# Kernel tuning notes

Measured on AMD Instinct MI355X. Metric: run time of the kernel, lower is better.

Reference implementation:

```python
import jax, jax.numpy as jnp
import numpy as np

B, N, C = 64, 256, 1024
H = 16
D = C // H            # head_dim = 64
HALF = D // 2         # rope dim per axis = 32
PT = 16               # hw_seq_len
THETA = 10000.0


def build_rope_tables():
    # VisionRotaryEmbeddingFast: per-axis freqs, repeated r=2, 2D broadcat
    freqs = 1.0 / (THETA ** (np.arange(0, HALF, 2, dtype=np.float32) / HALF))  # [HALF/2]=16
    t = np.arange(PT, dtype=np.float32)                                        # ft==pt -> t=arange
    f = t[:, None] * freqs[None, :]                                            # [16,16]
    f = np.repeat(f, 2, axis=-1)                                               # [16,32]
    f2d = np.concatenate(
        [np.broadcast_to(f[:, None, :], (PT, PT, HALF)),
         np.broadcast_to(f[None, :, :], (PT, PT, HALF))], axis=-1)             # [16,16,64]
    f2d = f2d.reshape(PT * PT, D)                                              # [256,64]
    return jnp.asarray(np.cos(f2d)), jnp.asarray(np.sin(f2d))


def rotate_half(t):
    # (..., d) -> pairwise (x0,x1) -> (-x1, x0)
    t2 = t.reshape(*t.shape[:-1], -1, 2)
    return jnp.stack([-t2[..., 1], t2[..., 0]], axis=-1).reshape(t.shape)


def apply_rope(t, cos, sin):
    # t: [B,H,N,D]; cos/sin: [N,D]
    return t * cos + rotate_half(t) * sin


def setup_inputs() -> dict:
    key = jax.random.key(0)
    k1, k2, k3 = jax.random.split(key, 3)
    x = jax.random.normal(k1, (B, N, C), dtype=jnp.float32)
    mask = jnp.ones((1, 1, N, N), dtype=bool)  # True = attend (SDPA bool mask)
    qkv_w = jax.random.normal(k2, (3 * C, C), dtype=jnp.float32) * 0.02
    qkv_b = jnp.zeros((3 * C,), dtype=jnp.float32)
    proj_w = jax.random.normal(k3, (C, C), dtype=jnp.float32) * 0.02
    proj_b = jnp.zeros((C,), dtype=jnp.float32)
    rope_cos, rope_sin = build_rope_tables()
    return {"x": x, "mask": mask, "qkv_w": qkv_w, "qkv_b": qkv_b,
            "proj_w": proj_w, "proj_b": proj_b,
            "rope_cos": rope_cos, "rope_sin": rope_sin}


def reference(x, mask, qkv_w, qkv_b, proj_w, proj_b, rope_cos, rope_sin):
    b, n, c = x.shape
    scale = 1.0 / jnp.sqrt(jnp.asarray(D, x.dtype))
    qkv = x @ qkv_w.T + qkv_b                              # [B,N,3C]
    qkv = qkv.reshape(b, n, 3, H, D).transpose(2, 0, 3, 1, 4)  # [3,B,H,N,D]
    q, k, v = qkv[0], qkv[1], qkv[2]
    q = apply_rope(q, rope_cos, rope_sin)
    k = apply_rope(k, rope_cos, rope_sin)
    scores = jnp.einsum('bhnd,bhmd->bhnm', q, k) * scale   # [B,H,N,N]
    neg = jnp.asarray(jnp.finfo(scores.dtype).min, scores.dtype)
    scores = jnp.where(mask, scores, neg)
    attn = jax.nn.softmax(scores, axis=-1)
    out = jnp.einsum('bhnm,bhmd->bhnd', attn, v)           # [B,H,N,D]
    out = out.transpose(0, 2, 1, 3).reshape(b, n, c)       # [B,N,C]
    return out @ proj_w.T + proj_b
```

## Files before the change

### kernel.cpp

```cpp
#include <hip/hip_runtime.h>
#include <math.h>

typedef short s16x8 __attribute__((ext_vector_type(8)));
typedef float f32x4 __attribute__((ext_vector_type(4)));

#define DEV static __device__ __forceinline__

DEV unsigned short f2bf(float f){
  unsigned int u = __builtin_bit_cast(unsigned int, f);
  u += 0x7fffu + ((u >> 16) & 1u);
  return (unsigned short)(u >> 16);
}

DEV void gload_lds16(const void* g, void* l){
  __builtin_amdgcn_global_load_lds(
      (const __attribute__((address_space(1))) unsigned int*)g,
      (__attribute__((address_space(3))) unsigned int*)l,
      16, 0, 0);
}

DEV void stage_tile(const short* __restrict__ g, short* lds, int ld, int row0, int k0, int tid){
#pragma unroll
  for (int issue = 0; issue < 2; ++issue){
    int fi  = issue*256 + tid;
    int row = fi >> 2;
    int c8  = (fi & 3) * 8;
    const short* ga = g + (size_t)(row0 + row)*ld + k0 + c8;
    short* lb = lds + (size_t)(issue*256 + (tid & ~63))*8;
    gload_lds16(ga, lb);
  }
}

__global__ void cvt_bf16(const float* __restrict__ in, short* __restrict__ out, int n8){
  int i = blockIdx.x*blockDim.x + threadIdx.x;
  if (i >= n8) return;
  const float* p = in + (size_t)i*8;
  f32x4 a = *(const f32x4*)(p);
  f32x4 b = *(const f32x4*)(p+4);
  s16x8 o;
#pragma unroll
  for (int j=0;j<4;++j){ o[j] = (short)f2bf(a[j]); o[4+j] = (short)f2bf(b[j]); }
  *(s16x8*)(out + (size_t)i*8) = o;
}

template<int EPI>
__global__ __launch_bounds__(256)
void gemm_bt(const short* __restrict__ A, const short* __restrict__ Bw,
             const float* __restrict__ bias,
             const float* __restrict__ cosT, const float* __restrict__ sinT,
             short* __restrict__ q_out, short* __restrict__ k_out, short* __restrict__ v_out,
             float* __restrict__ f_out)
{
  constexpr int K = 1024;
  constexpr int NT = K/32;
  __shared__ short As[2][128*32];
  __shared__ short Bs[2][128*32];
  const int tid  = threadIdx.x;
  const int lane = tid & 63;
  const int wid  = tid >> 6;
  const int n0 = blockIdx.x * 128;
  const int m0 = blockIdx.y * 128;
  const int wr = (wid >> 1) * 64;
  const int wc = (wid & 1) * 64;
  const int lr = lane & 15;
  const int lk = lane >> 4;

  stage_tile(A,  As[0], K, m0, 0, tid);
  stage_tile(Bw, Bs[0], K, n0, 0, tid);
  asm volatile("s_waitcnt vmcnt(0)" ::: "memory");
  __syncthreads();

  f32x4 acc[4][4] = {};
  int cur = 0;
  for (int kt = 0; kt < NT; ++kt){
    if (kt + 1 < NT){
      stage_tile(A,  As[cur^1], K, m0, (kt+1)*32, tid);
      stage_tile(Bw, Bs[cur^1], K, n0, (kt+1)*32, tid);
    }
    s16x8 af[4], bf[4];
#pragma unroll
    for (int mi=0; mi<4; ++mi)
      af[mi] = *(const s16x8*)&As[cur][(wr + mi*16 + lr)*32 + lk*8];
#pragma unroll
    for (int ni=0; ni<4; ++ni)
      bf[ni] = *(const s16x8*)&Bs[cur][(wc + ni*16 + lr)*32 + lk*8];
#pragma unroll
    for (int mi=0; mi<4; ++mi)
#pragma unroll
      for (int ni=0; ni<4; ++ni)
        acc[mi][ni] = __builtin_amdgcn_mfma_f32_16x16x32_bf16(af[mi], bf[ni], acc[mi][ni], 0, 0, 0);
    asm volatile("s_waitcnt vmcnt(0)" ::: "memory");
    __syncthreads();
    cur ^= 1;
  }

  if constexpr (EPI == 0){
    const int sel = n0 >> 10;
#pragma unroll
    for (int mi=0; mi<4; ++mi){
#pragma unroll
      for (int ni=0; ni<4; ++ni){
        const int col  = n0 + wc + ni*16 + lr;
        const int rowb = m0 + wr + mi*16 + lk*4;
        const float bv = bias[col];
        const int rem = col & 1023;
        const int h = rem >> 6, d = rem & 63;
        if (sel < 2){
          short* dst = (sel == 0) ? q_out : k_out;
#pragma unroll
          for (int r=0; r<4; ++r){
            const int m = rowb + r;
            const int n = m & 255, b = m >> 8;
            float v = acc[mi][ni][r] + bv;
            float partner = __shfl_xor(v, 1, 64);
            float rot = (lane & 1) ? partner : -partner;
            float o = v * cosT[n*64 + d] + rot * sinT[n*64 + d];
            if (sel == 0) o *= 0.125f;
            dst[(((size_t)b*16 + h)*256 + n)*64 + d] = (short)f2bf(o);
          }
        } else {
          const int m = rowb;
          const int n = m & 255, b = m >> 8;
          unsigned long long pk = 0;
#pragma unroll
          for (int r=0; r<4; ++r)
            pk |= ((unsigned long long)f2bf(acc[mi][ni][r] + bv)) << (16*r);
          *(unsigned long long*)(v_out + (((size_t)b*16 + h)*64 + d)*256 + n) = pk;
        }
      }
    }
  } else {
#pragma unroll
    for (int mi=0; mi<4; ++mi){
#pragma unroll
      for (int ni=0; ni<4; ++ni){
        const int col  = n0 + wc + ni*16 + lr;
        const int rowb = m0 + wr + mi*16 + lk*4;
        const float bv = bias[col];
#pragma unroll
        for (int r=0; r<4; ++r)
          f_out[(size_t)(rowb + r)*1024 + col] = acc[mi][ni][r] + bv;
      }
    }
  }
}

__global__ __launch_bounds__(512)
void attn_kernel(const short* __restrict__ qh, const short* __restrict__ kh,
                 const short* __restrict__ vt, short* __restrict__ ao)
{
  __shared__ short Ks[256*64];
  __shared__ short Vs[64*256];
  __shared__ short Ps[8][32*64];
  const int tid  = threadIdx.x;
  const int lane = tid & 63;
  const int wid  = tid >> 6;
  const int lr   = lane & 15;
  const int lk   = lane >> 4;
  const int bh = blockIdx.x;
  const size_t base = (size_t)bh * 256 * 64;
  const short* Kg = kh + base;
  const short* Qg = qh + base;
  const short* Vg = vt + base;

#pragma unroll
  for (int p=0; p<4; ++p){
    int flat = (p*512 + tid)*8;
    uint4 kv = *(const uint4*)(Kg + flat);
    int krow = flat >> 6;  int kcb = (flat & 63)*2;
    *(uint4*)((char*)Ks + krow*128 + (kcb ^ ((krow&7)<<4))) = kv;
    uint4 vv = *(const uint4*)(Vg + flat);
    int vrow = flat >> 8;  int vcb = (flat & 255)*2;
    *(uint4*)((char*)Vs + vrow*512 + (vcb ^ ((vrow&7)<<4))) = vv;
  }

  const int qbase = wid*32;
  s16x8 qf[2][2];
#pragma unroll
  for (int qr=0; qr<2; ++qr)
#pragma unroll
    for (int ks=0; ks<2; ++ks)
      qf[qr][ks] = *(const s16x8*)(Qg + (size_t)(qbase + qr*16 + lr)*64 + ks*32 + lk*8);

  __syncthreads();

  float mrun[2][4], lrun[2][4];
  f32x4 o[2][4] = {};
#pragma unroll
  for (int qr=0; qr<2; ++qr)
#pragma unroll
    for (int r=0; r<4; ++r){ mrun[qr][r] = -INFINITY; lrun[qr][r] = 0.f; }

  for (int t=0; t<4; ++t){
    f32x4 s[2][4] = {};
#pragma unroll
    for (int kc=0; kc<4; ++kc){
      const int row = t*64 + kc*16 + lr;
#pragma unroll
      for (int ks=0; ks<2; ++ks){
        const int cb = ks*64 + lk*16;
        s16x8 kf = *(const s16x8*)((char*)Ks + row*128 + (cb ^ ((row&7)<<4)));
#pragma unroll
        for (int qr=0; qr<2; ++qr)
          s[qr][kc] = __builtin_amdgcn_mfma_f32_16x16x32_bf16(qf[qr][ks], kf, s[qr][kc], 0, 0, 0);
      }
    }
#pragma unroll
    for (int qr=0; qr<2; ++qr)
#pragma unroll
      for (int r=0; r<4; ++r){
        float mx = fmaxf(fmaxf(s[qr][0][r], s[qr][1][r]), fmaxf(s[qr][2][r], s[qr][3][r]));
        mx = fmaxf(mx, __shfl_xor(mx, 1, 64));
        mx = fmaxf(mx, __shfl_xor(mx, 2, 64));
        mx = fmaxf(mx, __shfl_xor(mx, 4, 64));
        mx = fmaxf(mx, __shfl_xor(mx, 8, 64));
        const float mnew  = fmaxf(mrun[qr][r], mx);
        const float alpha = __expf(mrun[qr][r] - mnew);
        float rsum = 0.f;
#pragma unroll
        for (int kc=0; kc<4; ++kc){
          float p = __expf(s[qr][kc][r] - mnew);
          s[qr][kc][r] = p;
          rsum += p;
        }
        rsum += __shfl_xor(rsum, 1, 64);
        rsum += __shfl_xor(rsum, 2, 64);
        rsum += __shfl_xor(rsum, 4, 64);
        rsum += __shfl_xor(rsum, 8, 64);
        lrun[qr][r] = lrun[qr][r]*alpha + rsum;
        mrun[qr][r] = mnew;
#pragma unroll
        for (int oc=0; oc<4; ++oc) o[qr][oc][r] *= alpha;
      }
#pragma unroll
    for (int qr=0; qr<2; ++qr)
#pragma unroll
      for (int kc=0; kc<4; ++kc)
#pragma unroll
        for (int r=0; r<4; ++r){
          const int row = qr*16 + lk*4 + r;
          const int cb  = (kc*16 + lr)*2;
          *(short*)((char*)&Ps[wid][0] + row*128 + (cb ^ ((row&7)<<4))) = (short)f2bf(s[qr][kc][r]);
        }
#pragma unroll
    for (int ks2=0; ks2<2; ++ks2){
      s16x8 pf[2];
#pragma unroll
      for (int qr=0; qr<2; ++qr){
        const int row = qr*16 + lr;
        const int cb  = ks2*64 + lk*16;
        pf[qr] = *(const s16x8*)((char*)&Ps[wid][0] + row*128 + (cb ^ ((row&7)<<4)));
      }
#pragma unroll
      for (int oc=0; oc<4; ++oc){
        const int vrow = oc*16 + lr;
        const int vcb  = t*128 + ks2*64 + lk*16;
        s16x8 vf = *(const s16x8*)((char*)Vs + vrow*512 + (vcb ^ ((vrow&7)<<4)));
#pragma unroll
        for (int qr=0; qr<2; ++qr)
          o[qr][oc] = __builtin_amdgcn_mfma_f32_16x16x32_bf16(pf[qr], vf, o[qr][oc], 0, 0, 0);
      }
    }
  }

  const int b = bh >> 4, h = bh & 15;
#pragma unroll
  for (int qr=0; qr<2; ++qr)
#pragma unroll
    for (int oc=0; oc<4; ++oc)
#pragma unroll
      for (int r=0; r<4; ++r){
        const int n = qbase + qr*16 + lk*4 + r;
        const int d = oc*16 + lr;
        float val = o[qr][oc][r] / lrun[qr][r];
        ao[(size_t)(b*256 + n)*1024 + h*64 + d] = (short)f2bf(val);
      }
}

extern "C" void kernel_launch(void* const* d_in, const int* in_sizes, int n_in,
                              void* d_out, int out_size, void* d_ws, size_t ws_size,
                              hipStream_t stream)
{
  const float* x      = (const float*)d_in[0];
  const float* qkv_w  = (const float*)d_in[2];
  const float* qkv_b  = (const float*)d_in[3];
  const float* proj_w = (const float*)d_in[4];
  const float* proj_b = (const float*)d_in[5];
  const float* rc     = (const float*)d_in[6];
  const float* rs     = (const float*)d_in[7];

  char* ws = (char*)d_ws;
  short* xbf   = (short*)(ws);
  short* wqkv  = (short*)(ws + 33554432);
  short* wproj = (short*)(ws + 39845888);
  short* qhb   = (short*)(ws + 41943040);
  short* khb   = (short*)(ws + 75497472);
  short* vtb   = (short*)(ws + 109051904);
  short* aob   = xbf;

  cvt_bf16<<<8192, 256, 0, stream>>>(x,      xbf,   2097152);
  cvt_bf16<<<1536, 256, 0, stream>>>(qkv_w,  wqkv,   393216);
  cvt_bf16<<< 512, 256, 0, stream>>>(proj_w, wproj,  131072);

  gemm_bt<0><<<dim3(24,128), 256, 0, stream>>>(xbf, wqkv, qkv_b, rc, rs,
                                               qhb, khb, vtb, nullptr);
  attn_kernel<<<1024, 512, 0, stream>>>(qhb, khb, vtb, aob);
  gemm_bt<1><<<dim3(8,128), 256, 0, stream>>>(aob, wproj, proj_b, nullptr, nullptr,
                                              nullptr, nullptr, nullptr, (float*)d_out);
}
```

Measured before the change: 420.7 us.

## Rewrite GEMMs with 256x128 tiles, triple-buffered swizzled LDS, and grouped block order

Replaces the 128x128, double-buffered, 256-thread GEMM with a 512-thread kernel. It uses 256x128 tiles, BK=64, and a three-stage global_load_lds pipeline with partial vmcnt waits. LDS rows are XOR-swizzled to avoid bank conflicts, the block index is remapped for L2 locality, and priority is raised around the MFMA bursts. The aim is to hide global load latency and raise MFMA utilization in both the QKV and projection GEMMs. The cost is 144KB of LDS per block, which limits occupancy, and more complex barrier logic.

```diff
diff --git a/kernel.cpp b/kernel.cpp
--- a/kernel.cpp
+++ b/kernel.cpp
@@ -17,18 +17,6 @@
       (const __attribute__((address_space(1))) unsigned int*)g,
       (__attribute__((address_space(3))) unsigned int*)l,
       16, 0, 0);
-}
-
-DEV void stage_tile(const short* __restrict__ g, short* lds, int ld, int row0, int k0, int tid){
-#pragma unroll
-  for (int issue = 0; issue < 2; ++issue){
-    int fi  = issue*256 + tid;
-    int row = fi >> 2;
-    int c8  = (fi & 3) * 8;
-    const short* ga = g + (size_t)(row0 + row)*ld + k0 + c8;
-    short* lb = lds + (size_t)(issue*256 + (tid & ~63))*8;
-    gload_lds16(ga, lb);
-  }
 }
 
 __global__ void cvt_bf16(const float* __restrict__ in, short* __restrict__ out, int n8){
@@ -44,102 +32,144 @@
 }
 
 template<int EPI>
-__global__ __launch_bounds__(256)
-void gemm_bt(const short* __restrict__ A, const short* __restrict__ Bw,
+DEV void stage_half(const short* __restrict__ Ag, const short* __restrict__ Bg,
+                    char* buf, int m0, int n0, int k0, int wid, int lane, int half){
+  const int l8 = lane >> 3, l7 = lane & 7;
+  const int cole = ((l7 ^ l8) << 3) + k0;
+#pragma unroll
+  for (int j = 0; j < 2; ++j){
+    const int chunk = (half*2 + j)*8 + wid;
+    const short* src = Ag + (size_t)(m0 + chunk*8 + l8)*1024 + cole;
+    gload_lds16(src, buf + chunk*1024);
+  }
+  {
+    const int chunk = half*8 + wid;
+    const short* src = Bg + (size_t)(n0 + chunk*8 + l8)*1024 + cole;
+    gload_lds16(src, buf + 32768 + chunk*1024);
+  }
+}
+
+template<int EPI>
+__global__ __launch_bounds__(512, 2)
+void gemm_dp(const short* __restrict__ A, const short* __restrict__ Bw,
              const float* __restrict__ bias,
              const float* __restrict__ cosT, const float* __restrict__ sinT,
              short* __restrict__ q_out, short* __restrict__ k_out, short* __restrict__ v_out,
              float* __restrict__ f_out)
 {
-  constexpr int K = 1024;
-  constexpr int NT = K/32;
-  __shared__ short As[2][128*32];
-  __shared__ short Bs[2][128*32];
+  constexpr int K  = 1024;
+  constexpr int BK = 64;
+  constexpr int NT = K / BK;
+  constexpr int NX = (EPI == 0) ? 24 : 8;
+  constexpr int TB = 49152;
+  __shared__ char smem[3 * TB];
+
   const int tid  = threadIdx.x;
   const int lane = tid & 63;
   const int wid  = tid >> 6;
-  const int n0 = blockIdx.x * 128;
-  const int m0 = blockIdx.y * 128;
-  const int wr = (wid >> 1) * 64;
-  const int wc = (wid & 1) * 64;
-  const int lr = lane & 15;
-  const int lk = lane >> 4;
-
-  stage_tile(A,  As[0], K, m0, 0, tid);
-  stage_tile(Bw, Bs[0], K, n0, 0, tid);
+  const int wm   = wid >> 2;
+  const int wn   = wid & 3;
+  const int lr   = lane & 15;
+  const int lk   = lane >> 4;
+
+  const int nwg = NX * 64;
+  const int bid = blockIdx.x;
+  const int swz = (bid & 7) * (nwg >> 3) + (bid >> 3);
+  const int mt  = swz & 63;
+  const int nt  = swz >> 6;
+  const int m0  = mt * 256;
+  const int n0  = nt * 128;
+
+  char* b0 = smem;
+  char* b1 = smem + TB;
+  char* b2 = smem + 2*TB;
+
+  stage_half<EPI>(A, Bw, b0, m0, n0, 0,  wid, lane, 0);
+  stage_half<EPI>(A, Bw, b0, m0, n0, 0,  wid, lane, 1);
+  stage_half<EPI>(A, Bw, b1, m0, n0, BK, wid, lane, 0);
+  stage_half<EPI>(A, Bw, b1, m0, n0, BK, wid, lane, 1);
+  asm volatile("s_waitcnt vmcnt(6)" ::: "memory");
+  asm volatile("s_barrier" ::: "memory");
+
+  f32x4 acc[8][2] = {};
+
+  for (int t = 0; t < NT; ++t){
+    const int ks = (t + 2 < NT ? (t + 2) : (NT - 1)) * BK;
+#pragma unroll
+    for (int kk = 0; kk < 2; ++kk){
+      s16x8 af[8], bf[2];
+      const int cb = kk*64 + lk*16;
+#pragma unroll
+      for (int m = 0; m < 8; ++m){
+        const int row = wm*128 + m*16 + lr;
+        af[m] = *(const s16x8*)(b0 + row*128 + (cb ^ ((row & 7) << 4)));
+      }
+#pragma unroll
+      for (int n = 0; n < 2; ++n){
+        const int row = wn*32 + n*16 + lr;
+        bf[n] = *(const s16x8*)(b0 + 32768 + row*128 + (cb ^ ((row & 7) << 4)));
+      }
+      stage_half<EPI>(A, Bw, b2, m0, n0, ks, wid, lane, kk);
+      asm volatile("s_barrier" ::: "memory");
+      __builtin_amdgcn_s_setprio(1);
+#pragma unroll
+      for (int m = 0; m < 8; ++m)
+#pragma unroll
+        for (int n = 0; n < 2; ++n)
+          acc[m][n] = __builtin_amdgcn_mfma_f32_16x16x32_bf16(af[m], bf[n], acc[m][n], 0, 0, 0);
+      __builtin_amdgcn_s_setprio(0);
+    }
+    asm volatile("s_waitcnt vmcnt(6)" ::: "memory");
+    asm volatile("s_barrier" ::: "memory");
+    char* tmp = b0; b0 = b1; b1 = b2; b2 = tmp;
+  }
   asm volatile("s_waitcnt vmcnt(0)" ::: "memory");
-  __syncthreads();
-
-  f32x4 acc[4][4] = {};
-  int cur = 0;
-  for (int kt = 0; kt < NT; ++kt){
-    if (kt + 1 < NT){
-      stage_tile(A,  As[cur^1], K, m0, (kt+1)*32, tid);
-      stage_tile(Bw, Bs[cur^1], K, n0, (kt+1)*32, tid);
-    }
-    s16x8 af[4], bf[4];
-#pragma unroll
-    for (int mi=0; mi<4; ++mi)
-      af[mi] = *(const s16x8*)&As[cur][(wr + mi*16 + lr)*32 + lk*8];
-#pragma unroll
-    for (int ni=0; ni<4; ++ni)
-      bf[ni] = *(const s16x8*)&Bs[cur][(wc + ni*16 + lr)*32 + lk*8];
-#pragma unroll
-    for (int mi=0; mi<4; ++mi)
-#pragma unroll
-      for (int ni=0; ni<4; ++ni)
-        acc[mi][ni] = __builtin_amdgcn_mfma_f32_16x16x32_bf16(af[mi], bf[ni], acc[mi][ni], 0, 0, 0);
-    asm volatile("s_waitcnt vmcnt(0)" ::: "memory");
-    __syncthreads();
-    cur ^= 1;
-  }
 
   if constexpr (EPI == 0){
     const int sel = n0 >> 10;
-#pragma unroll
-    for (int mi=0; mi<4; ++mi){
-#pragma unroll
-      for (int ni=0; ni<4; ++ni){
-        const int col  = n0 + wc + ni*16 + lr;
-        const int rowb = m0 + wr + mi*16 + lk*4;
+    short* dst0 = (sel == 0) ? q_out : k_out;
+#pragma unroll
+    for (int m = 0; m < 8; ++m){
+#pragma unroll
+      for (int n = 0; n < 2; ++n){
+        const int col  = n0 + wn*32 + n*16 + lr;
+        const int rowb = m0 + wm*128 + m*16 + lk*4;
         const float bv = bias[col];
         const int rem = col & 1023;
         const int h = rem >> 6, d = rem & 63;
         if (sel < 2){
-          short* dst = (sel == 0) ? q_out : k_out;
-#pragma unroll
-          for (int r=0; r<4; ++r){
-            const int m = rowb + r;
-            const int n = m & 255, b = m >> 8;
-            float v = acc[mi][ni][r] + bv;
+#pragma unroll
+          for (int r = 0; r < 4; ++r){
+            const int row = rowb + r;
+            const int ntok = row & 255, b = row >> 8;
+            float v = acc[m][n][r] + bv;
             float partner = __shfl_xor(v, 1, 64);
             float rot = (lane & 1) ? partner : -partner;
-            float o = v * cosT[n*64 + d] + rot * sinT[n*64 + d];
+            float o = v * cosT[ntok*64 + d] + rot * sinT[ntok*64 + d];
             if (sel == 0) o *= 0.125f;
-            dst[(((size_t)b*16 + h)*256 + n)*64 + d] = (short)f2bf(o);
+            dst0[(((size_t)b*16 + h)*256 + ntok)*64 + d] = (short)f2bf(o);
           }
         } else {
-          const int m = rowb;
-          const int n = m & 255, b = m >> 8;
+          const int ntok = rowb & 255, b = rowb >> 8;
           unsigned long long pk = 0;
 #pragma unroll
-          for (int r=0; r<4; ++r)
-            pk |= ((unsigned long long)f2bf(acc[mi][ni][r] + bv)) << (16*r);
-          *(unsigned long long*)(v_out + (((size_t)b*16 + h)*64 + d)*256 + n) = pk;
+          for (int r = 0; r < 4; ++r)
+            pk |= ((unsigned long long)f2bf(acc[m][n][r] + bv)) << (16*r);
+          *(unsigned long long*)(v_out + (((size_t)b*16 + h)*64 + d)*256 + ntok) = pk;
         }
       }
     }
   } else {
 #pragma unroll
-    for (int mi=0; mi<4; ++mi){
-#pragma unroll
-      for (int ni=0; ni<4; ++ni){
-        const int col  = n0 + wc + ni*16 + lr;
-        const int rowb = m0 + wr + mi*16 + lk*4;
+    for (int m = 0; m < 8; ++m){
+#pragma unroll
+      for (int n = 0; n < 2; ++n){
+        const int col  = n0 + wn*32 + n*16 + lr;
+        const int rowb = m0 + wm*128 + m*16 + lk*4;
         const float bv = bias[col];
 #pragma unroll
-        for (int r=0; r<4; ++r)
-          f_out[(size_t)(rowb + r)*1024 + col] = acc[mi][ni][r] + bv;
+        for (int r = 0; r < 4; ++r)
+          f_out[(size_t)(rowb + r)*1024 + col] = acc[m][n][r] + bv;
       }
     }
   }
@@ -302,9 +332,9 @@
   cvt_bf16<<<1536, 256, 0, stream>>>(qkv_w,  wqkv,   393216);
   cvt_bf16<<< 512, 256, 0, stream>>>(proj_w, wproj,  131072);
 
-  gemm_bt<0><<<dim3(24,128), 256, 0, stream>>>(xbf, wqkv, qkv_b, rc, rs,
-                                               qhb, khb, vtb, nullptr);
+  gemm_dp<0><<<1536, 512, 0, stream>>>(xbf, wqkv, qkv_b, rc, rs,
+                                       qhb, khb, vtb, nullptr);
   attn_kernel<<<1024, 512, 0, stream>>>(qhb, khb, vtb, aob);
-  gemm_bt<1><<<dim3(8,128), 256, 0, stream>>>(aob, wproj, proj_b, nullptr, nullptr,
-                                              nullptr, nullptr, nullptr, (float*)d_out);
-}
+  gemm_dp<1><<<512, 512, 0, stream>>>(aob, wproj, proj_b, nullptr, nullptr,
+                                      nullptr, nullptr, nullptr, (float*)d_out);
+}
```

Result: slower. 440.6 us (+4.7%).
